# Optimization experiments

Hardware: AMD Instinct MI355X
Metric: run time of the kernel (lower is better)

The kernel has to match this reference:

```python
import jax, jax.numpy as jnp
import numpy as np

B, S, D, H = 4, 2048, 512, 8
DEPTH = D // H


def setup_inputs() -> dict:
    key = jax.random.key(0)
    ks = jax.random.split(key, 12)
    scale = 0.02
    inp = {
        "q": jax.random.normal(ks[0], (B, S, D), dtype=jnp.float32),
        "k": jax.random.normal(ks[1], (B, S, D), dtype=jnp.float32),
        "v": jax.random.normal(ks[2], (B, S, D), dtype=jnp.float32),
        "mask": jax.random.randint(ks[3], (B, S, S), 0, 2, dtype=jnp.int32),
        "wq": jax.random.normal(ks[4], (D, D), dtype=jnp.float32) * scale,
        "bq": jnp.zeros((D,), dtype=jnp.float32),
        "wk": jax.random.normal(ks[5], (D, D), dtype=jnp.float32) * scale,
        "bk": jnp.zeros((D,), dtype=jnp.float32),
        "wv": jax.random.normal(ks[6], (D, D), dtype=jnp.float32) * scale,
        "bv": jnp.zeros((D,), dtype=jnp.float32),
        "wo": jax.random.normal(ks[7], (D, D), dtype=jnp.float32) * scale,
        "bo": jnp.zeros((D,), dtype=jnp.float32),
    }
    return inp


def _split_heads(x):
    # [B, S, D] -> [B, H, S, depth]
    b, s, _ = x.shape
    return x.reshape(b, s, H, DEPTH).transpose(0, 2, 1, 3)


def reference(q, k, v, mask, wq, bq, wk, bk, wv, bv, wo, bo):
    qh = _split_heads(q @ wq + bq)
    kh = _split_heads(k @ wk + bk)
    vh = _split_heads(v @ wv + bv)
    # scaled dot-product attention with additive mask, materializing [B,H,S,S]
    scores = jnp.einsum("bhqd,bhkd->bhqk", qh, kh) / jnp.sqrt(
        jnp.asarray(DEPTH, jnp.float32)
    )
    scores = scores + mask[:, None, :, :].astype(jnp.float32) * (-1e9)
    w = jax.nn.softmax(scores, axis=-1)
    o = jnp.einsum("bhqk,bhkd->bhqd", w, vh)
    o = o.transpose(0, 2, 1, 3).reshape(q.shape[0], -1, D)  # [B, S, D]
    return o @ wo + bo
```

## Files before the change

kernel.cpp:

```cpp
#include <hip/hip_runtime.h>
#include <hip/hip_bf16.h>
#include <stdint.h>

#define B_ 4
#define S_ 2048
#define D_ 512
#define H_ 8

typedef __attribute__((ext_vector_type(8))) short short8;
typedef __attribute__((ext_vector_type(4))) short short4v;
typedef __attribute__((ext_vector_type(4))) float f32x4;
typedef __attribute__((ext_vector_type(4))) unsigned short u16x4;

#define MFMA16(a,b,c) __builtin_amdgcn_mfma_f32_16x16x32_bf16((a),(b),(c),0,0,0)
#define MFMA16K(a,b,c) __builtin_amdgcn_mfma_f32_16x16x16bf16_1k((a),(b),(c),0,0,0)

#if __has_builtin(__builtin_amdgcn_sbfe)
#define SBFE1(v, off) ((uint32_t)__builtin_amdgcn_sbfe((int)(v), (off), 1))
#else
#define SBFE1(v, off) ((uint32_t)(((int32_t)((v) << (31-(off)))) >> 31))
#endif

__device__ __forceinline__ unsigned short f2bf(float f){
    return __builtin_bit_cast(unsigned short, __float2bfloat16(f));
}

__device__ __forceinline__ float maskf(float p, uint32_t keep){
    return __builtin_bit_cast(float, __builtin_bit_cast(uint32_t, p) & keep);
}

__device__ __forceinline__ float max3f(float a, float b, float c){
    float d;
    asm("v_max3_f32 %0, %1, %2, %3" : "=v"(d) : "v"(a), "v"(b), "v"(c));
    return d;
}

__device__ __forceinline__ void gload_lds16(const void* g, void* l){
    __builtin_amdgcn_global_load_lds((const __attribute__((address_space(1))) uint32_t*)g,
                                     (__attribute__((address_space(3))) uint32_t*)l, 16, 0, 0);
}

__global__ __launch_bounds__(256) void prep_kernel(
    const float* __restrict__ wq, const float* __restrict__ wk,
    const float* __restrict__ wv, const float* __restrict__ wo,
    unsigned short* __restrict__ wt)
{
    int f = blockIdx.x*256 + threadIdx.x;
    int mat = f >> 18;
    int rem = f & 262143;
    const float* Wm = (mat==0)?wq:(mat==1)?wk:(mat==2)?wv:wo;
    int kk = rem >> 9, nn = rem & 511;
    wt[(size_t)mat*262144 + (size_t)nn*512 + kk] = f2bf(Wm[rem]);
}

__global__ __launch_bounds__(256) void proj_kernel(
    const float* __restrict__ q, const float* __restrict__ k, const float* __restrict__ v,
    const float* __restrict__ bq, const float* __restrict__ bk, const float* __restrict__ bv,
    const unsigned short* __restrict__ wt, unsigned short* __restrict__ outb,
    const int* __restrict__ mask, uint32_t* __restrict__ mout)
{
    __shared__ uint8_t smem[32768];
    const int t = threadIdx.x, l = t&63, w = t>>6, g = l>>4, ln = l&15;
    const int z = blockIdx.z;

    if (z >= 3){
        int seg = (z-3)*256 + blockIdx.y*64 + blockIdx.x;
        int idx = seg*256 + t;
        const int4* p = (const int4*)(mask + (size_t)idx*32);
        uint32_t bits = 0;
        #pragma unroll
        for (int c=0;c<8;c++){
            int4 vv = p[c];
            if (vv.x) bits |= 1u << (c*4+0);
            if (vv.y) bits |= 1u << (c*4+1);
            if (vv.z) bits |= 1u << (c*4+2);
            if (vv.w) bits |= 1u << (c*4+3);
        }
        mout[idx] = bits;
        return;
    }

    const float* X = (z==0)? q : (z==1)? k : v;
    const float* bias = (z==0)? bq : (z==1)? bk : bv;
    const unsigned short* WTz = wt + (size_t)z*(D_*D_);
    unsigned short* out = outb + (size_t)z*((size_t)B_*H_*S_*64);
    const float scale = (z==0)? 0.18033688011112042f : 1.0f;
    const int m0 = blockIdx.x*128, n0 = blockIdx.y*128;
    uint8_t* As = smem; uint8_t* Bs = smem + 16384;
    const int RB = (w>>1)*64, CB = (w&1)*64;

    const f32x4 zz = {0.f,0.f,0.f,0.f};
    f32x4 acc[4][4];
    #pragma unroll
    for (int i=0;i<4;i++)
        #pragma unroll
        for (int j=0;j<4;j++) acc[i][j] = zz;

    for (int k0=0; k0<D_; k0+=64){
        __syncthreads();
        #pragma unroll
        for (int i=0;i<4;i++){
            int qc = w + i*4;
            int row = qc*8 + (l>>3);
            int colb = ((l&7)*16) ^ ((row&7)<<4);
            gload_lds16((const uint8_t*)WTz + (((size_t)(n0+row)*D_ + k0)<<1) + colb,
                        Bs + qc*1024);
        }
        #pragma unroll
        for (int i=0;i<4;i++){
            int c = t + i*256;
            int row = c>>3, cc = c&7;
            const float4* src = (const float4*)(X + (size_t)(m0+row)*D_ + k0 + cc*8);
            float4 u0 = src[0], u1 = src[1];
            uint32_t c0,c1,c2,c3;
            asm("v_cvt_pk_bf16_f32 %0, %1, %2" : "=v"(c0) : "v"(u0.x), "v"(u0.y));
            asm("v_cvt_pk_bf16_f32 %0, %1, %2" : "=v"(c1) : "v"(u0.z), "v"(u0.w));
            asm("v_cvt_pk_bf16_f32 %0, %1, %2" : "=v"(c2) : "v"(u1.x), "v"(u1.y));
            asm("v_cvt_pk_bf16_f32 %0, %1, %2" : "=v"(c3) : "v"(u1.z), "v"(u1.w));
            uint4 pk4; pk4.x=c0; pk4.y=c1; pk4.z=c2; pk4.w=c3;
            *(uint4*)(As + row*128 + ((cc*16) ^ ((row&7)<<4))) = pk4;
        }
        __syncthreads();
        #pragma unroll
        for (int kc=0; kc<2; kc++){
            short8 af[4], bfr[4];
            #pragma unroll
            for (int ai=0; ai<4; ai++){
                int row = RB + 16*ai + ln;
                af[ai] = *(const short8*)(As + row*128 + ((16*g + 64*kc) ^ ((row&7)<<4)));
            }
            #pragma unroll
            for (int bj=0; bj<4; bj++){
                int row = CB + 16*bj + ln;
                bfr[bj] = *(const short8*)(Bs + row*128 + ((16*g + 64*kc) ^ ((row&7)<<4)));
            }
            if (z == 2){
                #pragma unroll
                for (int ai=0; ai<4; ai++)
                    #pragma unroll
                    for (int bj=0; bj<4; bj++)
                        acc[ai][bj] = MFMA16(bfr[bj], af[ai], acc[ai][bj]);
            } else {
                #pragma unroll
                for (int ai=0; ai<4; ai++)
                    #pragma unroll
                    for (int bj=0; bj<4; bj++)
                        acc[ai][bj] = MFMA16(af[ai], bfr[bj], acc[ai][bj]);
            }
        }
    }

    if (z == 2){
        const int lnperm = 8*(ln>>2) + (ln&3);
        const int bidx = m0 >> 11;
        const int schunk = (m0 + RB) & 2047;
        #pragma unroll
        for (int bj=0; bj<4; bj++){
            #pragma unroll
            for (int ai=0; ai<4; ai++){
                int soff = schunk + 32*(ai>>1) + 4*(ai&1) + lnperm;
                #pragma unroll
                for (int r=0;r<4;r++){
                    int gn = n0 + CB + 16*bj + 4*g + r;
                    float val = acc[ai][bj][r] + bias[gn];
                    out[((size_t)bidx*D_ + gn)*S_ + soff] = f2bf(val);
                }
            }
        }
    } else {
        #pragma unroll
        for (int bj=0; bj<4; bj++){
            int gn = n0 + CB + 16*bj + ln;
            float bv2 = bias[gn];
            int h = gn >> 6, dep = gn & 63;
            #pragma unroll
            for (int ai=0; ai<4; ai++){
                #pragma unroll
                for (int r=0;r<4;r++){
                    int gm = m0 + RB + 16*ai + 4*g + r;
                    float val = (acc[ai][bj][r] + bv2) * scale;
                    size_t o = ((size_t)(gm>>11)*H_ + h)*((size_t)S_*64) + (size_t)(gm&2047)*64 + dep;
                    out[o] = f2bf(val);
                }
            }
        }
    }
}

__global__ __launch_bounds__(256, 4) void attn_kernel(
    const unsigned short* __restrict__ qb, const unsigned short* __restrict__ kb,
    const unsigned short* __restrict__ vtb, const uint32_t* __restrict__ mb,
    unsigned short* __restrict__ ao)
{
    __shared__ uint8_t smem[32768];
    const int t = threadIdx.x, l = t&63, w = t>>6, g = l>>4, ln = l&15;
    const int fid = blockIdx.x + 32*blockIdx.y;
    const int slot = fid >> 3;
    const int bh = (fid & 7) + 8*(slot >> 5);
    const int q0 = (slot & 31) * 64;
    const int b = bh >> 3;
    const unsigned short* Q  = qb + (size_t)bh*((size_t)S_*64);
    const unsigned short* K  = kb + (size_t)bh*((size_t)S_*64);
    const unsigned short* VT = vtb + ((size_t)b*D_ + (bh&7)*64)*S_;

    const int qrow = q0 + 16*w + ln;
    const short8 qf0 = *(const short8*)(Q + (size_t)qrow*64 + 8*g);
    const short8 qf1 = *(const short8*)(Q + (size_t)qrow*64 + 8*g + 32);

    const int Msw = (ln&7)<<4;
    const int sw0 = (16*g) ^ Msw;
    const int sw1 = (16*g + 64) ^ Msw;
    uint8_t* kB0 = smem + ln*128 + sw0;
    uint8_t* kB1 = smem + ln*128 + sw1;
    uint8_t* vB  = smem + 16384 + ln*128;
    const int vpo0 = (16*g     ) ^ Msw;
    const int vpo1 = (16*g + 64) ^ Msw;

    int krow0 = w*8 + (l>>3), krow1 = (w+4)*8 + (l>>3);
    int colb0 = ((l&7)*16) ^ ((krow0&7)<<4);
    int colb1 = ((l&7)*16) ^ ((krow1&7)<<4);
    int kof0 = krow0*128 + colb0,     kof1 = krow1*128 + colb1;
    int vof0 = krow0*(S_*2) + colb0,  vof1 = krow1*(S_*2) + colb1;
    const int ldo0 = w*1024, ldo1 = (w+4)*1024;

    const uint2* mptr = (const uint2*)(mb + ((size_t)b*S_ + qrow)*64);

    const f32x4 zz = {0.f,0.f,0.f,0.f};
    f32x4 O[4], O5 = zz;
    #pragma unroll
    for (int i=0;i<4;i++) O[i] = zz;
    float c = 0.f;

    const short4v onesv = {0x3F80,0x3F80,0x3F80,0x3F80};

    gload_lds16((const uint8_t*)K  + kof0, smem + ldo0);
    gload_lds16((const uint8_t*)K  + kof1, smem + ldo1);
    gload_lds16((const uint8_t*)VT + vof0, smem + 16384 + ldo0);
    gload_lds16((const uint8_t*)VT + vof1, smem + 16384 + ldo1);
    kof0 += 8192; kof1 += 8192; vof0 += 128; vof1 += 128;
    int curb = 0;
    uint2 mmc = mptr[0];

    for (int it=0; it<S_/64; ++it){
        __syncthreads();
        if (it < S_/64 - 1){
            int nx = curb ^ 8192;
            gload_lds16((const uint8_t*)K  + kof0, smem + nx + ldo0);
            gload_lds16((const uint8_t*)K  + kof1, smem + nx + ldo1);
            gload_lds16((const uint8_t*)VT + vof0, smem + 16384 + nx + ldo0);
            gload_lds16((const uint8_t*)VT + vof1, smem + 16384 + nx + ldo1);
            kof0 += 8192; kof1 += 8192; vof0 += 128; vof1 += 128;
        }
        uint2 mmn = mptr[(it+1)&31];
        const uint8_t* b0 = kB0 + curb;
        const uint8_t* b1 = kB1 + curb;

        f32x4 st[4];
        __builtin_amdgcn_s_setprio(1);
        #pragma unroll
        for (int t4=0;t4<4;t4++){
            short8 kf0 = *(const short8*)(b0 + 2048*t4);
            short8 kf1 = *(const short8*)(b1 + 2048*t4);
            st[t4] = MFMA16(kf0, qf0, zz);
            st[t4] = MFMA16(kf1, qf1, st[t4]);
        }
        __builtin_amdgcn_s_setprio(0);

        float m0a = max3f(st[0][0], st[0][1], st[0][2]);
        float m1a = max3f(st[0][3], st[1][0], st[1][1]);
        float m2a = max3f(st[1][2], st[1][3], st[2][0]);
        float m3a = max3f(st[2][1], st[2][2], st[2][3]);
        float m4a = max3f(st[3][0], st[3][1], st[3][2]);
        float lmax = fmaxf(max3f(m0a, m1a, m2a), max3f(m3a, m4a, st[3][3]));
        if (__builtin_expect(__any(lmax > c + 8.0f), 0)){
            float rm = lmax;
            rm = fmaxf(rm, __shfl_xor(rm, 16));
            rm = fmaxf(rm, __shfl_xor(rm, 32));
            float cnew = fmaxf(c, rm);
            float al = __builtin_amdgcn_exp2f(c - cnew);
            c = cnew;
            #pragma unroll
            for (int r=0;r<4;r++){
                float aO = __shfl(al, 4*g + r);
                #pragma unroll
                for (int db=0; db<4; db++) O[db][r] *= aO;
                O5[r] *= aO;
            }
        }

        uint32_t mi0 = (~mmc.x) >> (4*g);
        uint32_t mi1 = (~mmc.y) >> (4*g);
        short4v pa[4];
        auto genp = [&](float cc){
            #pragma unroll
            for (int t4=0;t4<4;t4++){
                uint32_t mi = (t4 >= 2) ? mi1 : mi0;
                const int base = (t4&1)*16;
                float p0 = maskf(__builtin_amdgcn_exp2f(st[t4][0] - cc), SBFE1(mi, base+0));
                float p1 = maskf(__builtin_amdgcn_exp2f(st[t4][1] - cc), SBFE1(mi, base+1));
                float p2 = maskf(__builtin_amdgcn_exp2f(st[t4][2] - cc), SBFE1(mi, base+2));
                float p3 = maskf(__builtin_amdgcn_exp2f(st[t4][3] - cc), SBFE1(mi, base+3));
                uint32_t lo, hi;
                asm("v_cvt_pk_bf16_f32 %0, %1, %2" : "=v"(lo) : "v"(p0), "v"(p1));
                asm("v_cvt_pk_bf16_f32 %0, %1, %2" : "=v"(hi) : "v"(p2), "v"(p3));
                uint2 u; u.x = lo; u.y = hi;
                pa[t4] = __builtin_bit_cast(short4v, u);
            }
        };
        if (__builtin_expect(__all(c == 0.0f), 1)) genp(0.0f); else genp(c);
        mmc = mmn;

        __builtin_amdgcn_s_setprio(1);
        const uint8_t* vb = vB + curb;
        #pragma unroll
        for (int db=0; db<4; db++){
            short8 vp0 = *(const short8*)(vb + 2048*db + vpo0);
            short8 vp1 = *(const short8*)(vb + 2048*db + vpo1);
            short4v vf0 = {vp0[0],vp0[1],vp0[2],vp0[3]};
            short4v vf1 = {vp0[4],vp0[5],vp0[6],vp0[7]};
            short4v vf2 = {vp1[0],vp1[1],vp1[2],vp1[3]};
            short4v vf3 = {vp1[4],vp1[5],vp1[6],vp1[7]};
            O[db] = MFMA16K(pa[0], vf0, O[db]);
            O[db] = MFMA16K(pa[1], vf1, O[db]);
            O[db] = MFMA16K(pa[2], vf2, O[db]);
            O[db] = MFMA16K(pa[3], vf3, O[db]);
        }
        O5 = MFMA16K(pa[0], onesv, O5);
        O5 = MFMA16K(pa[1], onesv, O5);
        O5 = MFMA16K(pa[2], onesv, O5);
        O5 = MFMA16K(pa[3], onesv, O5);
        __builtin_amdgcn_s_setprio(0);
        curb ^= 8192;
    }

    #pragma unroll
    for (int r=0;r<4;r++){
        float inv = 1.0f / O5[r];
        int gm = b*S_ + q0 + 16*w + 4*g + r;
        #pragma unroll
        for (int db=0; db<4; db++){
            int col = (bh&7)*64 + 16*db + ln;
            ao[(size_t)gm*D_ + col] = f2bf(O[db][r]*inv);
        }
    }
}

__global__ __launch_bounds__(256) void outproj_kernel(
    const unsigned short* __restrict__ ao, const unsigned short* __restrict__ wt,
    const float* __restrict__ bo, float* __restrict__ out)
{
    __shared__ uint8_t smem[24576];
    const int t = threadIdx.x, l = t&63, w = t>>6, g = l>>4, ln = l&15;
    const unsigned short* WTz = wt + (size_t)3*(D_*D_);
    const int m0 = blockIdx.x*128, n0 = blockIdx.y*64;
    uint8_t* As = smem; uint8_t* Bs = smem + 16384;
    const int RB = (w>>1)*64, CB = (w&1)*32;

    const f32x4 zz = {0.f,0.f,0.f,0.f};
    f32x4 acc[4][2];
    #pragma unroll
    for (int i=0;i<4;i++)
        #pragma unroll
        for (int j=0;j<2;j++) acc[i][j] = zz;

    for (int k0=0; k0<D_; k0+=64){
        __syncthreads();
        #pragma unroll
        for (int i=0;i<2;i++){
            int qc = w + i*4;
            int row = qc*8 + (l>>3);
            int colb = ((l&7)*16) ^ ((row&7)<<4);
            gload_lds16((const uint8_t*)WTz + (((size_t)(n0+row)*D_ + k0)<<1) + colb,
                        Bs + qc*1024);
        }
        #pragma unroll
        for (int i=0;i<4;i++){
            int qc = w + i*4;
            int row = qc*8 + (l>>3);
            int colb = ((l&7)*16) ^ ((row&7)<<4);
            gload_lds16((const uint8_t*)ao + (((size_t)(m0+row)*D_ + k0)<<1) + colb,
                        As + qc*1024);
        }
        __syncthreads();
        #pragma unroll
        for (int kc=0; kc<2; kc++){
            short8 af[4], bfr[2];
            #pragma unroll
            for (int ai=0; ai<4; ai++){
                int row = RB + 16*ai + ln;
                af[ai] = *(const short8*)(As + row*128 + ((16*g + 64*kc) ^ ((row&7)<<4)));
            }
            #pragma unroll
            for (int bj=0; bj<2; bj++){
                int row = CB + 16*bj + ln;
                bfr[bj] = *(const short8*)(Bs + row*128 + ((16*g + 64*kc) ^ ((row&7)<<4)));
            }
            #pragma unroll
            for (int ai=0; ai<4; ai++)
                #pragma unroll
                for (int bj=0; bj<2; bj++)
                    acc[ai][bj] = MFMA16(af[ai], bfr[bj], acc[ai][bj]);
        }
    }

    #pragma unroll
    for (int bj=0; bj<2; bj++){
        int gn = n0 + CB + 16*bj + ln;
        float bv2 = bo[gn];
        #pragma unroll
        for (int ai=0; ai<4; ai++){
            #pragma unroll
            for (int r=0;r<4;r++){
                int gm = m0 + RB + 16*ai + 4*g + r;
                out[(size_t)gm*D_ + gn] = acc[ai][bj][r] + bv2;
            }
        }
    }
}

extern "C" void kernel_launch(void* const* d_in, const int* in_sizes, int n_in,
                              void* d_out, int out_size, void* d_ws, size_t ws_size,
                              hipStream_t stream)
{
    const float* q  = (const float*)d_in[0];
    const float* k  = (const float*)d_in[1];
    const float* v  = (const float*)d_in[2];
    const int* mask = (const int*)d_in[3];
    const float* wq = (const float*)d_in[4];
    const float* bq = (const float*)d_in[5];
    const float* wk = (const float*)d_in[6];
    const float* bk = (const float*)d_in[7];
    const float* wv = (const float*)d_in[8];
    const float* bv = (const float*)d_in[9];
    const float* wo = (const float*)d_in[10];
    const float* bo = (const float*)d_in[11];

    uint8_t* ws = (uint8_t*)d_ws;
    unsigned short* qkvb = (unsigned short*)ws;
    unsigned short* ao   = (unsigned short*)(ws + 25165824);
    unsigned short* wt   = (unsigned short*)(ws + 33554432);
    uint32_t*       mb   = (uint32_t*)      (ws + 35651584);
    float* out = (float*)d_out;

    prep_kernel<<<dim3(4096), dim3(256), 0, stream>>>(wq, wk, wv, wo, wt);
    proj_kernel<<<dim3(64,4,11), dim3(256), 0, stream>>>(q, k, v, bq, bk, bv, wt, qkvb, mask, mb);
    attn_kernel<<<dim3(32,32), dim3(256), 0, stream>>>(qkvb, qkvb + 4194304, qkvb + 8388608, mb, ao);
    outproj_kernel<<<dim3(64,8), dim3(256), 0, stream>>>(ao, wt, bo, out);
}
```

Baseline: 114.2 us.

## Rewrite attention with 32x32x16 MFMA tiles and two-wave blocks

Switches the attention kernel from 16x16 MFMA tiles with four waves to 32x32x16 bf16 MFMA with two waves per block, each wave owning 32 query rows. The row sum is now kept by explicit register accumulation instead of an extra ones-vector MFMA, and P fragments are repacked with v_permlane32_swap. Rescale factors and the final normalisation pass through a small LDS scratch area. The V^T store layout in the projection kernel changes to plain sequence order to match. The aim is fewer MFMA issues and fewer LDS reads per FLOP, at the cost of more registers per wave and fewer waves per block to hide latency.

Result: slower. 117.5 us (+2.9%).

```diff
diff --git a/kernel.cpp b/kernel.cpp
--- a/kernel.cpp
+++ b/kernel.cpp
@@ -8,12 +8,11 @@
 #define H_ 8
 
 typedef __attribute__((ext_vector_type(8))) short short8;
-typedef __attribute__((ext_vector_type(4))) short short4v;
 typedef __attribute__((ext_vector_type(4))) float f32x4;
-typedef __attribute__((ext_vector_type(4))) unsigned short u16x4;
+typedef __attribute__((ext_vector_type(16))) float f32x16;
 
 #define MFMA16(a,b,c) __builtin_amdgcn_mfma_f32_16x16x32_bf16((a),(b),(c),0,0,0)
-#define MFMA16K(a,b,c) __builtin_amdgcn_mfma_f32_16x16x16bf16_1k((a),(b),(c),0,0,0)
+#define MFMA32(a,b,c) __builtin_amdgcn_mfma_f32_32x32x16_bf16((a),(b),(c),0,0,0)
 
 #if __has_builtin(__builtin_amdgcn_sbfe)
 #define SBFE1(v, off) ((uint32_t)__builtin_amdgcn_sbfe((int)(v), (off), 1))
@@ -151,19 +150,16 @@
     }
 
     if (z == 2){
-        const int lnperm = 8*(ln>>2) + (ln&3);
-        const int bidx = m0 >> 11;
-        const int schunk = (m0 + RB) & 2047;
         #pragma unroll
         for (int bj=0; bj<4; bj++){
             #pragma unroll
             for (int ai=0; ai<4; ai++){
-                int soff = schunk + 32*(ai>>1) + 4*(ai&1) + lnperm;
+                int s = m0 + RB + 16*ai + ln;
                 #pragma unroll
                 for (int r=0;r<4;r++){
                     int gn = n0 + CB + 16*bj + 4*g + r;
                     float val = acc[ai][bj][r] + bias[gn];
-                    out[((size_t)bidx*D_ + gn)*S_ + soff] = f2bf(val);
+                    out[((size_t)(s>>11)*D_ + gn)*S_ + (s&2047)] = f2bf(val);
                 }
             }
         }
@@ -187,13 +183,14 @@
     }
 }
 
-__global__ __launch_bounds__(256, 4) void attn_kernel(
+__global__ __launch_bounds__(128, 2) void attn_kernel(
     const unsigned short* __restrict__ qb, const unsigned short* __restrict__ kb,
     const unsigned short* __restrict__ vtb, const uint32_t* __restrict__ mb,
     unsigned short* __restrict__ ao)
 {
-    __shared__ uint8_t smem[32768];
-    const int t = threadIdx.x, l = t&63, w = t>>6, g = l>>4, ln = l&15;
+    __shared__ uint8_t smem[33024];
+    const int t = threadIdx.x, l = t&63, wv = t>>6;
+    const int q31 = l&31, hi = l>>5;
     const int fid = blockIdx.x + 32*blockIdx.y;
     const int slot = fid >> 3;
     const int bh = (fid & 7) + 8*(slot >> 5);
@@ -203,41 +200,43 @@
     const unsigned short* K  = kb + (size_t)bh*((size_t)S_*64);
     const unsigned short* VT = vtb + ((size_t)b*D_ + (bh&7)*64)*S_;
 
-    const int qrow = q0 + 16*w + ln;
-    const short8 qf0 = *(const short8*)(Q + (size_t)qrow*64 + 8*g);
-    const short8 qf1 = *(const short8*)(Q + (size_t)qrow*64 + 8*g + 32);
-
-    const int Msw = (ln&7)<<4;
-    const int sw0 = (16*g) ^ Msw;
-    const int sw1 = (16*g + 64) ^ Msw;
-    uint8_t* kB0 = smem + ln*128 + sw0;
-    uint8_t* kB1 = smem + ln*128 + sw1;
-    uint8_t* vB  = smem + 16384 + ln*128;
-    const int vpo0 = (16*g     ) ^ Msw;
-    const int vpo1 = (16*g + 64) ^ Msw;
-
-    int krow0 = w*8 + (l>>3), krow1 = (w+4)*8 + (l>>3);
-    int colb0 = ((l&7)*16) ^ ((krow0&7)<<4);
-    int colb1 = ((l&7)*16) ^ ((krow1&7)<<4);
-    int kof0 = krow0*128 + colb0,     kof1 = krow1*128 + colb1;
-    int vof0 = krow0*(S_*2) + colb0,  vof1 = krow1*(S_*2) + colb1;
-    const int ldo0 = w*1024, ldo1 = (w+4)*1024;
+    const int qrow = q0 + 32*wv + q31;
+    short8 qf[4];
+    #pragma unroll
+    for (int kc=0;kc<4;kc++)
+        qf[kc] = *(const short8*)(Q + (size_t)qrow*64 + 16*kc + 8*hi);
+
+    const int rowb = q31*128;
+    int osw[4];
+    #pragma unroll
+    for (int kc=0;kc<4;kc++)
+        osw[kc] = rowb + ((32*kc + 16*hi) ^ ((l&7)<<4));
+
+    int kof[4], vof[4], ldo[4];
+    #pragma unroll
+    for (int i=0;i<4;i++){
+        int qc = wv + 2*i;
+        int row = qc*8 + (l>>3);
+        int colb = ((l&7)*16) ^ ((row&7)<<4);
+        kof[i] = row*128 + colb;
+        vof[i] = row*(S_*2) + colb;
+        ldo[i] = qc*1024;
+    }
 
     const uint2* mptr = (const uint2*)(mb + ((size_t)b*S_ + qrow)*64);
-
-    const f32x4 zz = {0.f,0.f,0.f,0.f};
-    f32x4 O[4], O5 = zz;
-    #pragma unroll
-    for (int i=0;i<4;i++) O[i] = zz;
-    float c = 0.f;
-
-    const short4v onesv = {0x3F80,0x3F80,0x3F80,0x3F80};
-
-    gload_lds16((const uint8_t*)K  + kof0, smem + ldo0);
-    gload_lds16((const uint8_t*)K  + kof1, smem + ldo1);
-    gload_lds16((const uint8_t*)VT + vof0, smem + 16384 + ldo0);
-    gload_lds16((const uint8_t*)VT + vof1, smem + 16384 + ldo1);
-    kof0 += 8192; kof1 += 8192; vof0 += 128; vof1 += 128;
+    float* epl = (float*)(smem + 32768 + wv*128);
+
+    f32x16 O0, O1, z16;
+    #pragma unroll
+    for (int i=0;i<16;i++){ O0[i]=0.f; O1[i]=0.f; z16[i]=0.f; }
+    float c = 0.f, lsum = 0.f;
+
+    #pragma unroll
+    for (int i=0;i<4;i++){
+        gload_lds16((const uint8_t*)K  + kof[i], smem + ldo[i]);
+        gload_lds16((const uint8_t*)VT + vof[i], smem + 16384 + ldo[i]);
+        kof[i] += 8192; vof[i] += 128;
+    }
     int curb = 0;
     uint2 mmc = mptr[0];
 
@@ -245,103 +244,110 @@
         __syncthreads();
         if (it < S_/64 - 1){
             int nx = curb ^ 8192;
-            gload_lds16((const uint8_t*)K  + kof0, smem + nx + ldo0);
-            gload_lds16((const uint8_t*)K  + kof1, smem + nx + ldo1);
-            gload_lds16((const uint8_t*)VT + vof0, smem + 16384 + nx + ldo0);
-            gload_lds16((const uint8_t*)VT + vof1, smem + 16384 + nx + ldo1);
-            kof0 += 8192; kof1 += 8192; vof0 += 128; vof1 += 128;
+            #pragma unroll
+            for (int i=0;i<4;i++){
+                gload_lds16((const uint8_t*)K  + kof[i], smem + nx + ldo[i]);
+                gload_lds16((const uint8_t*)VT + vof[i], smem + 16384 + nx + ldo[i]);
+                kof[i] += 8192; vof[i] += 128;
+            }
         }
         uint2 mmn = mptr[(it+1)&31];
-        const uint8_t* b0 = kB0 + curb;
-        const uint8_t* b1 = kB1 + curb;
-
-        f32x4 st[4];
+
+        const uint8_t* kbp = smem + curb;
+        f32x16 st0 = z16, st1 = z16;
         __builtin_amdgcn_s_setprio(1);
         #pragma unroll
-        for (int t4=0;t4<4;t4++){
-            short8 kf0 = *(const short8*)(b0 + 2048*t4);
-            short8 kf1 = *(const short8*)(b1 + 2048*t4);
-            st[t4] = MFMA16(kf0, qf0, zz);
-            st[t4] = MFMA16(kf1, qf1, st[t4]);
+        for (int kc=0;kc<4;kc++){
+            short8 kf0 = *(const short8*)(kbp + osw[kc]);
+            short8 kf1 = *(const short8*)(kbp + osw[kc] + 4096);
+            st0 = MFMA32(kf0, qf[kc], st0);
+            st1 = MFMA32(kf1, qf[kc], st1);
         }
         __builtin_amdgcn_s_setprio(0);
 
-        float m0a = max3f(st[0][0], st[0][1], st[0][2]);
-        float m1a = max3f(st[0][3], st[1][0], st[1][1]);
-        float m2a = max3f(st[1][2], st[1][3], st[2][0]);
-        float m3a = max3f(st[2][1], st[2][2], st[2][3]);
-        float m4a = max3f(st[3][0], st[3][1], st[3][2]);
-        float lmax = fmaxf(max3f(m0a, m1a, m2a), max3f(m3a, m4a, st[3][3]));
-        if (__builtin_expect(__any(lmax > c + 8.0f), 0)){
-            float rm = lmax;
-            rm = fmaxf(rm, __shfl_xor(rm, 16));
-            rm = fmaxf(rm, __shfl_xor(rm, 32));
+        float mx = max3f(st0[0], st0[1], st0[2]);
+        #pragma unroll
+        for (int i=3;i<15;i+=2) mx = max3f(mx, st0[i], st0[i+1]);
+        mx = fmaxf(mx, st0[15]);
+        #pragma unroll
+        for (int i=0;i<15;i+=2) mx = max3f(mx, st1[i], st1[i+1]);
+        mx = fmaxf(mx, st1[15]);
+        if (__builtin_expect(__any(mx > c + 8.0f), 0)){
+            float rm = fmaxf(mx, __shfl_xor(mx, 32));
             float cnew = fmaxf(c, rm);
             float al = __builtin_amdgcn_exp2f(c - cnew);
             c = cnew;
-            #pragma unroll
-            for (int r=0;r<4;r++){
-                float aO = __shfl(al, 4*g + r);
-                #pragma unroll
-                for (int db=0; db<4; db++) O[db][r] *= aO;
-                O5[r] *= aO;
-            }
-        }
-
-        uint32_t mi0 = (~mmc.x) >> (4*g);
-        uint32_t mi1 = (~mmc.y) >> (4*g);
-        short4v pa[4];
+            lsum *= al;
+            if (l < 32) epl[q31] = al;
+            asm volatile("s_waitcnt lgkmcnt(0)" ::: "memory");
+            #pragma unroll
+            for (int r=0;r<16;r++){
+                float ar = epl[(r&3) + 8*(r>>2) + 4*hi];
+                O0[r] *= ar; O1[r] *= ar;
+            }
+        }
+
+        uint32_t mi0 = (~mmc.x) >> (4*hi);
+        uint32_t mi1 = (~mmc.y) >> (4*hi);
+        float p0[16], p1[16];
         auto genp = [&](float cc){
             #pragma unroll
-            for (int t4=0;t4<4;t4++){
-                uint32_t mi = (t4 >= 2) ? mi1 : mi0;
-                const int base = (t4&1)*16;
-                float p0 = maskf(__builtin_amdgcn_exp2f(st[t4][0] - cc), SBFE1(mi, base+0));
-                float p1 = maskf(__builtin_amdgcn_exp2f(st[t4][1] - cc), SBFE1(mi, base+1));
-                float p2 = maskf(__builtin_amdgcn_exp2f(st[t4][2] - cc), SBFE1(mi, base+2));
-                float p3 = maskf(__builtin_amdgcn_exp2f(st[t4][3] - cc), SBFE1(mi, base+3));
-                uint32_t lo, hi;
-                asm("v_cvt_pk_bf16_f32 %0, %1, %2" : "=v"(lo) : "v"(p0), "v"(p1));
-                asm("v_cvt_pk_bf16_f32 %0, %1, %2" : "=v"(hi) : "v"(p2), "v"(p3));
-                uint2 u; u.x = lo; u.y = hi;
-                pa[t4] = __builtin_bit_cast(short4v, u);
+            for (int r=0;r<16;r++){
+                int bit = 8*(r>>2) + (r&3);
+                p0[r] = maskf(__builtin_amdgcn_exp2f(st0[r] - cc), SBFE1(mi0, bit));
+                p1[r] = maskf(__builtin_amdgcn_exp2f(st1[r] - cc), SBFE1(mi1, bit));
             }
         };
         if (__builtin_expect(__all(c == 0.0f), 1)) genp(0.0f); else genp(c);
         mmc = mmn;
 
+        {
+            float s = 0.f;
+            #pragma unroll
+            for (int r=0;r<16;r++) s += p0[r] + p1[r];
+            lsum += s + __shfl_xor(s, 32);
+        }
+
+        short8 pa[4];
+        #pragma unroll
+        for (int c2=0;c2<4;c2++){
+            const float* pp = (c2>=2) ? p1 : p0;
+            int qa4 = 8*(c2&1);
+            uint32_t a0, a1, b0, b1;
+            asm("v_cvt_pk_bf16_f32 %0, %1, %2" : "=v"(a0) : "v"(pp[qa4+0]), "v"(pp[qa4+1]));
+            asm("v_cvt_pk_bf16_f32 %0, %1, %2" : "=v"(a1) : "v"(pp[qa4+2]), "v"(pp[qa4+3]));
+            asm("v_cvt_pk_bf16_f32 %0, %1, %2" : "=v"(b0) : "v"(pp[qa4+4]), "v"(pp[qa4+5]));
+            asm("v_cvt_pk_bf16_f32 %0, %1, %2" : "=v"(b1) : "v"(pp[qa4+6]), "v"(pp[qa4+7]));
+            asm volatile("v_permlane32_swap_b32 %0, %1" : "+v"(a0), "+v"(b0));
+            asm volatile("v_permlane32_swap_b32 %0, %1" : "+v"(a1), "+v"(b1));
+            uint4 u; u.x = a0; u.y = a1; u.z = b0; u.w = b1;
+            pa[c2] = __builtin_bit_cast(short8, u);
+        }
+
+        const uint8_t* vbp = smem + 16384 + curb;
         __builtin_amdgcn_s_setprio(1);
-        const uint8_t* vb = vB + curb;
-        #pragma unroll
-        for (int db=0; db<4; db++){
-            short8 vp0 = *(const short8*)(vb + 2048*db + vpo0);
-            short8 vp1 = *(const short8*)(vb + 2048*db + vpo1);
-            short4v vf0 = {vp0[0],vp0[1],vp0[2],vp0[3]};
-            short4v vf1 = {vp0[4],vp0[5],vp0[6],vp0[7]};
-            short4v vf2 = {vp1[0],vp1[1],vp1[2],vp1[3]};
-            short4v vf3 = {vp1[4],vp1[5],vp1[6],vp1[7]};
-            O[db] = MFMA16K(pa[0], vf0, O[db]);
-            O[db] = MFMA16K(pa[1], vf1, O[db]);
-            O[db] = MFMA16K(pa[2], vf2, O[db]);
-            O[db] = MFMA16K(pa[3], vf3, O[db]);
-        }
-        O5 = MFMA16K(pa[0], onesv, O5);
-        O5 = MFMA16K(pa[1], onesv, O5);
-        O5 = MFMA16K(pa[2], onesv, O5);
-        O5 = MFMA16K(pa[3], onesv, O5);
+        #pragma unroll
+        for (int c2=0;c2<4;c2++){
+            short8 vf0 = *(const short8*)(vbp + osw[c2]);
+            short8 vf1 = *(const short8*)(vbp + osw[c2] + 4096);
+            O0 = MFMA32(pa[c2], vf0, O0);
+            O1 = MFMA32(pa[c2], vf1, O1);
+        }
         __builtin_amdgcn_s_setprio(0);
         curb ^= 8192;
     }
 
-    #pragma unroll
-    for (int r=0;r<4;r++){
-        float inv = 1.0f / O5[r];
-        int gm = b*S_ + q0 + 16*w + 4*g + r;
-        #pragma unroll
-        for (int db=0; db<4; db++){
-            int col = (bh&7)*64 + 16*db + ln;
-            ao[(size_t)gm*D_ + col] = f2bf(O[db][r]*inv);
-        }
+    float inv = 1.0f / lsum;
+    if (l < 32) epl[q31] = inv;
+    asm volatile("s_waitcnt lgkmcnt(0)" ::: "memory");
+    const int colbase = (bh&7)*64 + q31;
+    #pragma unroll
+    for (int r=0;r<16;r++){
+        int qloc = (r&3) + 8*(r>>2) + 4*hi;
+        float ivr = epl[qloc];
+        size_t gm = (size_t)(b*S_ + q0 + 32*wv + qloc)*D_;
+        ao[gm + colbase     ] = f2bf(O0[r]*ivr);
+        ao[gm + colbase + 32] = f2bf(O1[r]*ivr);
     }
 }
 
@@ -444,6 +450,6 @@
 
     prep_kernel<<<dim3(4096), dim3(256), 0, stream>>>(wq, wk, wv, wo, wt);
     proj_kernel<<<dim3(64,4,11), dim3(256), 0, stream>>>(q, k, v, bq, bk, bv, wt, qkvb, mask, mb);
-    attn_kernel<<<dim3(32,32), dim3(256), 0, stream>>>(qkvb, qkvb + 4194304, qkvb + 8388608, mb, ao);
+    attn_kernel<<<dim3(32,32), dim3(128), 0, stream>>>(qkvb, qkvb + 4194304, qkvb + 8388608, mb, ao);
     outproj_kernel<<<dim3(64,8), dim3(256), 0, stream>>>(ao, wt, bo, out);
 }
```
